# Kernel tuning notes

Hardware: AMD Instinct MI355X
Metric: run time of the kernel (lower is better)

Reference implementation:

```python
import jax, jax.numpy as jnp
import numpy as np

D_MODEL, D_STATE, D_CONV, D_INNER, DT_RANK, K = 96, 16, 3, 192, 6, 4
B, H, W = 1, 64, 64


def setup_inputs() -> dict:
    key = jax.random.key(0)
    ks = jax.random.split(key, 10)
    x = jax.random.normal(ks[0], (B, H, W, D_MODEL), jnp.float32)
    in_proj_w = jax.random.normal(ks[1], (2 * D_INNER, D_MODEL), jnp.float32) * 0.02
    conv_w = jax.random.normal(ks[2], (D_INNER, 1, D_CONV, D_CONV), jnp.float32) * 0.1
    conv_b = jnp.zeros((D_INNER,), jnp.float32)
    x_proj_w = jax.random.normal(ks[3], (K, DT_RANK + 2 * D_STATE, D_INNER), jnp.float32) * 0.02
    dt_std = DT_RANK ** -0.5
    dt_w = jax.random.uniform(ks[4], (K, D_INNER, DT_RANK), jnp.float32, -dt_std, dt_std)
    # dt bias init: inv-softplus of dt ~ logUniform(1e-3, 1e-1)
    u = jax.random.uniform(ks[5], (K, D_INNER), jnp.float32)
    dt = jnp.exp(u * (np.log(0.1) - np.log(0.001)) + np.log(0.001)).clip(1e-4)
    dt_b = dt + jnp.log(-jnp.expm1(-dt))
    A_logs = jnp.log(jnp.broadcast_to(jnp.arange(1, D_STATE + 1, dtype=jnp.float32), (K * D_INNER, D_STATE)))
    Ds = jnp.ones((K * D_INNER,), jnp.float32)
    ln_g = jnp.ones((D_INNER,), jnp.float32)
    ln_b = jnp.zeros((D_INNER,), jnp.float32)
    out_proj_w = jax.random.normal(ks[6], (D_MODEL, D_INNER), jnp.float32) * 0.02
    return dict(x=x, in_proj_w=in_proj_w, conv_w=conv_w, conv_b=conv_b, x_proj_w=x_proj_w,
                dt_w=dt_w, dt_b=dt_b, A_logs=A_logs, Ds=Ds, ln_g=ln_g, ln_b=ln_b,
                out_proj_w=out_proj_w)


def _ss2d(x, in_proj_w, conv_w, conv_b, x_proj_w, dt_w, dt_b, A_logs, Ds, ln_g, ln_b, out_proj_w):
    b, h, w, c = x.shape
    L = h * w
    d = conv_w.shape[0]            # d_inner
    n = A_logs.shape[1]            # d_state
    r = dt_w.shape[2]              # dt_rank
    # in_proj + split
    xz = jnp.einsum('bhwc,ec->bhwe', x, in_proj_w)
    xx, z = xz[..., :d], xz[..., d:]
    # depthwise conv (NCHW) + SiLU
    xc = xx.transpose(0, 3, 1, 2)
    pad = (D_CONV - 1) // 2
    xc = jax.lax.conv_general_dilated(xc, conv_w, (1, 1), [(pad, pad), (pad, pad)],
                                      feature_group_count=d) + conv_b[None, :, None, None]
    xc = jax.nn.silu(xc)
    # 4 scan directions: HW, WH, and their reverses
    x_hw = xc.reshape(b, d, L)
    x_wh = xc.transpose(0, 1, 3, 2).reshape(b, d, L)
    xs = jnp.stack([x_hw, x_wh, x_hw[..., ::-1], x_wh[..., ::-1]], axis=1)  # (b,K,d,L)
    x_dbl = jnp.einsum('bkdl,kcd->bkcl', xs, x_proj_w)
    dts, Bs, Cs = x_dbl[:, :, :r], x_dbl[:, :, r:r + n], x_dbl[:, :, r + n:]
    dts = jnp.einsum('bkrl,kdr->bkdl', dts, dt_w)
    delta = jax.nn.softplus(dts + dt_b[None, :, :, None])        # (b,K,d,L)
    A = -jnp.exp(A_logs).reshape(K, d, n)
    # time-major scanned inputs
    dA = jnp.exp(jnp.einsum('bkdl,kdn->lbkdn', delta, A))        # (L,b,K,d,n)
    dBu = jnp.einsum('bkdl,bknl,bkdl->lbkdn', delta, Bs, xs)
    Ct = Cs.transpose(3, 0, 1, 2)                                # (L,b,K,n)
    def step(hst, inp):
        dA_t, dBu_t, C_t = inp
        hst = dA_t * hst + dBu_t
        return hst, jnp.einsum('bkdn,bkn->bkd', hst, C_t)
    h0 = jnp.zeros((b, K, d, n), jnp.float32)
    _, ys = jax.lax.scan(step, h0, (dA, dBu, Ct))                # ys: (L,b,K,d)
    out_y = ys.transpose(1, 2, 3, 0) + xs * Ds.reshape(K, d)[None, :, :, None]
    # recombine directions
    inv = out_y[:, 2:4][..., ::-1]
    y1 = out_y[:, 0]
    y2 = inv[:, 0]
    wh = out_y[:, 1].reshape(b, d, w, h).transpose(0, 1, 3, 2).reshape(b, d, L)
    invwh = inv[:, 1].reshape(b, d, w, h).transpose(0, 1, 3, 2).reshape(b, d, L)
    y = (y1 + y2 + wh + invwh).transpose(0, 2, 1).reshape(b, h, w, d)
    # LayerNorm (eps=1e-5, torch default)
    mu = y.mean(-1, keepdims=True)
    var = ((y - mu) ** 2).mean(-1, keepdims=True)
    y = (y - mu) * jax.lax.rsqrt(var + 1e-5) * ln_g + ln_b
    y = y * jax.nn.silu(z)
    return jnp.einsum('bhwd,cd->bhwc', y, out_proj_w)


def reference(x, in_proj_w, conv_w, conv_b, x_proj_w, dt_w, dt_b, A_logs, Ds, ln_g, ln_b, out_proj_w):
    return _ss2d(x, in_proj_w, conv_w, conv_b, x_proj_w, dt_w, dt_b, A_logs, Ds, ln_g, ln_b, out_proj_w)
```

## Files before the change

### kernel.cpp

```cpp
#include <hip/hip_runtime.h>
#include <hip/hip_bf16.h>

#define LL 4096
#define DM 96
#define DI 192
#define NS 16
#define RK 6
#define RKP 8
#define KD 4
#define CPROJ 38
#define NC (KD*DI*NS)
#define PT 32
#define WS 196
#define OT 16
#define L2E 1.44269504f

__device__ __forceinline__ float b2f(__hip_bfloat16 v){ return __bfloat162float(v); }

__device__ __forceinline__ int detect_bf16(const unsigned short* __restrict__ xh, int tid, int* sflag){
  if (tid < 64){
    unsigned short u = xh[2*tid];
    int e = (u >> 7) & 0xFF;
    int sane = (e >= 107 && e <= 131) ? 1 : 0;
    unsigned long long m = __ballot(sane);
    if (tid == 0) *sflag = (__popcll(m) >= 32) ? 1 : 0;
  }
  return 0;
}

struct P12 { const void* p[12]; };
__global__ void k_convert_all(P12 ptrs, float* __restrict__ dst) {
  const int off[13] = {0,393216,430080,431808,432000,461184,465792,466560,
                       478848,479616,479808,480000,498432};
  __shared__ int sflag;
  detect_bf16((const unsigned short*)ptrs.p[0], threadIdx.x, &sflag);
  __syncthreads();
  int f = sflag;
  int i = blockIdx.x * 256 + threadIdx.x;
  if (i >= 498432) return;
  int j = 0;
  #pragma unroll
  for (int s = 1; s < 12; s++) if (i >= off[s]) j = s;
  int e = i - off[j];
  if (f) dst[i] = b2f(((const __hip_bfloat16*)ptrs.p[j])[e]);
  else   dst[i] = ((const float*)ptrs.p[j])[e];
}

__global__ void k_inproj(const float* __restrict__ x,
                         const float* __restrict__ w,
                         float* __restrict__ xx, float* __restrict__ z) {
  __shared__ float xr[8*DM];
  int l0 = blockIdx.x * 8;
  int tid = threadIdx.x;
  for (int i = tid; i < 8*DM; i += 384) xr[i] = x[l0*DM + i];
  __syncthreads();
  int e = tid;
  float acc[8];
  #pragma unroll
  for (int i=0;i<8;i++) acc[i]=0.f;
  const float* wr = w + e*DM;
  for (int c=0;c<DM;c++){
    float wv = wr[c];
    #pragma unroll
    for (int i=0;i<8;i++) acc[i] = fmaf(wv, xr[i*DM+c], acc[i]);
  }
  if (e < DI) {
    #pragma unroll
    for (int i=0;i<8;i++) xx[(l0+i)*DI + e] = acc[i];
  } else {
    int e2 = e - DI;
    #pragma unroll
    for (int i=0;i<8;i++) z[(l0+i)*DI + e2] = acc[i];
  }
}

__global__ void k_conv(const float* __restrict__ xx,
                       const float* __restrict__ cw,
                       const float* __restrict__ cb,
                       float* __restrict__ xc) {
  int l = blockIdx.x;
  int d = threadIdx.x;
  int h = l >> 6, w = l & 63;
  float acc = cb[d];
  #pragma unroll
  for (int ki=0; ki<3; ki++){
    int hh = h + ki - 1;
    if ((unsigned)hh >= 64u) continue;
    #pragma unroll
    for (int kj=0;kj<3;kj++){
      int wj = w + kj - 1;
      if ((unsigned)wj >= 64u) continue;
      acc = fmaf(cw[d*9 + ki*3 + kj], xx[(hh*64+wj)*DI + d], acc);
    }
  }
  xc[l*DI + d] = acc / (1.f + __expf(-acc));
}

__device__ __forceinline__ int dir_map(int k, int t){
  if (k==0) return t;
  if (k==1) return ((t&63)<<6) | (t>>6);
  if (k==2) return 4095 - t;
  int u = 4095 - t; return ((u&63)<<6) | (u>>6);
}

__global__ void __launch_bounds__(256) k_proj(const float* __restrict__ xc,
                       const float* __restrict__ xpw,
                       float* __restrict__ dts,
                       float* __restrict__ Bb, float* __restrict__ Cb,
                       float* __restrict__ yacc) {
  __shared__ float wl[CPROJ*WS];
  __shared__ float xs[PT*WS];
  int b = blockIdx.x;
  int k = b >> 7;
  int t_base = (b & 127) * PT;
  int tid = threadIdx.x;
  if (k == 0){
    float4* yz = (float4*)(yacc + (size_t)t_base*DI);
    for (int idx = tid; idx < PT*DI/4; idx += 256)
      yz[idx] = make_float4(0.f,0.f,0.f,0.f);
  }
  for (int idx = tid; idx < CPROJ*DI; idx += 256){
    int cc = idx / DI, j = idx - cc*DI;
    wl[cc*WS + j] = xpw[(k*CPROJ + cc)*DI + j];
  }
  for (int idx = tid; idx < PT*DI; idx += 256){
    int tt = idx / DI, j = idx - tt*DI;
    xs[tt*WS + j] = xc[dir_map(k, t_base + tt)*DI + j];
  }
  __syncthreads();
  int tg = tid & 7;
  int ty = tid >> 3;
  int cc0 = ty;
  int has2 = (ty + 32 < CPROJ);
  int cc1 = has2 ? (ty + 32) : ty;
  float a0x=0.f,a0y=0.f,a0z=0.f,a0w=0.f;
  float a1x=0.f,a1y=0.f,a1z=0.f,a1w=0.f;
  const float4* w0p = (const float4*)&wl[cc0*WS];
  const float4* w1p = (const float4*)&wl[cc1*WS];
  const float4* x0p = (const float4*)&xs[(tg     )*WS];
  const float4* x1p = (const float4*)&xs[(tg +  8)*WS];
  const float4* x2p = (const float4*)&xs[(tg + 16)*WS];
  const float4* x3p = (const float4*)&xs[(tg + 24)*WS];
  #pragma unroll 4
  for (int jc = 0; jc < DI/4; jc++){
    float4 w0 = w0p[jc], w1 = w1p[jc];
    float4 x0 = x0p[jc], x1 = x1p[jc], x2 = x2p[jc], x3 = x3p[jc];
    a0x = fmaf(w0.x,x0.x,fmaf(w0.y,x0.y,fmaf(w0.z,x0.z,fmaf(w0.w,x0.w,a0x))));
    a0y = fmaf(w0.x,x1.x,fmaf(w0.y,x1.y,fmaf(w0.z,x1.z,fmaf(w0.w,x1.w,a0y))));
    a0z = fmaf(w0.x,x2.x,fmaf(w0.y,x2.y,fmaf(w0.z,x2.z,fmaf(w0.w,x2.w,a0z))));
    a0w = fmaf(w0.x,x3.x,fmaf(w0.y,x3.y,fmaf(w0.z,x3.z,fmaf(w0.w,x3.w,a0w))));
    a1x = fmaf(w1.x,x0.x,fmaf(w1.y,x0.y,fmaf(w1.z,x0.z,fmaf(w1.w,x0.w,a1x))));
    a1y = fmaf(w1.x,x1.x,fmaf(w1.y,x1.y,fmaf(w1.z,x1.z,fmaf(w1.w,x1.w,a1y))));
    a1z = fmaf(w1.x,x2.x,fmaf(w1.y,x2.y,fmaf(w1.z,x2.z,fmaf(w1.w,x2.w,a1z))));
    a1w = fmaf(w1.x,x3.x,fmaf(w1.y,x3.y,fmaf(w1.z,x3.z,fmaf(w1.w,x3.w,a1w))));
  }
  float accs0[4] = {a0x,a0y,a0z,a0w};
  float accs1[4] = {a1x,a1y,a1z,a1w};
  #pragma unroll
  for (int i=0;i<4;i++){
    int t = t_base + tg + 8*i;
    size_t kt = (size_t)k*LL + t;
    {
      int cc = cc0; float v = accs0[i];
      if (cc < RK)            dts[kt*RKP + cc] = v;
      else if (cc < RK+NS)    Bb [kt*NS + (cc-RK)] = v;
      else                    Cb [kt*NS + (cc-RK-NS)] = v;
    }
    if (has2){
      int cc = ty + 32; float v = accs1[i];
      if (cc < RK+NS)         Bb [kt*NS + (cc-RK)] = v;
      else                    Cb [kt*NS + (cc-RK-NS)] = v;
    }
  }
}

template<int CHB>
__global__ void __launch_bounds__(256) k_scan1(
                      const float* __restrict__ xc,
                      const float* __restrict__ dts,
                      const float* __restrict__ Bbuf,
                      const float* __restrict__ Cbuf,
                      const float* __restrict__ A_logs,
                      const float* __restrict__ dtw,
                      const float* __restrict__ dtb,
                      float* __restrict__ Pb, float* __restrict__ Hb,
                      float* __restrict__ SDb,
                      float* __restrict__ yacc) {
  constexpr int CS = LL >> CHB;
  int b = blockIdx.x;
  int c = b & ((1<<CHB)-1);
  int kg = b >> CHB;
  int k = kg / 3, dg3 = kg - k*3;
  int tid = threadIdx.x;
  int dl = tid >> 2, nq = tid & 3;
  int d = dg3*64 + dl;
  int kd = k*DI + d;
  float4 Al = *(const float4*)&A_logs[kd*NS + nq*4];
  float A0 = -__expf(Al.x)*L2E, A1 = -__expf(Al.y)*L2E;
  float A2 = -__expf(Al.z)*L2E, A3 = -__expf(Al.w)*L2E;
  float bt = dtb[kd];
  float w0 = dtw[kd*RK+0], w1 = dtw[kd*RK+1], w2 = dtw[kd*RK+2];
  float w3 = dtw[kd*RK+3], w4 = dtw[kd*RK+4], w5 = dtw[kd*RK+5];
  const float* dr = dts + ((size_t)k*LL + c*CS)*RKP;
  const float4* bp = (const float4*)(Bbuf + ((size_t)k*LL + c*CS)*NS) + nq;
  const float4* cp = (const float4*)(Cbuf + ((size_t)k*LL + c*CS)*NS) + nq;
  float h0=0.f,h1=0.f,h2=0.f,h3=0.f, cumD=0.f;
  for (int s=0; s<CS; s++){
    int t = c*CS + s;
    float4 lo = *(const float4*)(dr + s*RKP);
    float4 hi = *(const float4*)(dr + s*RKP + 4);
    float v = bt;
    v = fmaf(w0, lo.x, v); v = fmaf(w1, lo.y, v); v = fmaf(w2, lo.z, v);
    v = fmaf(w3, lo.w, v); v = fmaf(w4, hi.x, v); v = fmaf(w5, hi.y, v);
    float sp = (v > 20.f) ? v : __logf(1.f + __expf(v));
    cumD += sp;
    int l = dir_map(k,t);
    float sx = sp * xc[l*DI + d];
    float4 bv = bp[s*4];
    float4 cv = cp[s*4];
    float a;
    a = exp2f(sp*A0); h0 = fmaf(a, h0, sx*bv.x);
    a = exp2f(sp*A1); h1 = fmaf(a, h1, sx*bv.y);
    a = exp2f(sp*A2); h2 = fmaf(a, h2, sx*bv.z);
    a = exp2f(sp*A3); h3 = fmaf(a, h3, sx*bv.w);
    float y = h0*cv.x + h1*cv.y + h2*cv.z + h3*cv.w;
    y += __shfl_xor(y, 1, 64);
    y += __shfl_xor(y, 2, 64);
    if (nq == 0){
      atomicAdd(&yacc[(size_t)l*DI + d], y);
      SDb[(size_t)(k*LL + t)*DI + d] = cumD;
    }
  }
  int base = c*NC + kd*NS + nq*4;
  *(float4*)&Pb[base] = make_float4(exp2f(A0*cumD), exp2f(A1*cumD),
                                    exp2f(A2*cumD), exp2f(A3*cumD));
  *(float4*)&Hb[base] = make_float4(h0,h1,h2,h3);
}

__global__ void __launch_bounds__(256) k_scan2(
                      const float* __restrict__ Pb, float* __restrict__ Hb,
                      int CHn) {
  int idx = blockIdx.x*256 + threadIdx.x;
  float h = 0.f;
  #pragma unroll 4
  for (int c=0;c<CHn;c++){
    float P = Pb[c*NC + idx];
    float Hc = Hb[c*NC + idx];
    Hb[c*NC + idx] = h;
    h = fmaf(P, h, Hc);
  }
}

template<int CHB>
__global__ void __launch_bounds__(192) k_corr(
                      const float* __restrict__ Cbuf,
                      const float* __restrict__ A_logs,
                      const float* __restrict__ Hb,
                      const float* __restrict__ SDb,
                      float* __restrict__ yacc) {
  int b = blockIdx.x;
  int k = b >> 7;
  int t0 = (b & 127) * 32;
  int c = t0 >> (12 - CHB);
  if (c == 0) return;
  int d = threadIdx.x;
  int kd = k*DI + d;
  __shared__ float cs[32*NS];
  for (int i = d; i < 32*NS; i += 192)
    cs[i] = Cbuf[((size_t)k*LL + t0)*NS + i];
  float A2[16], he[16];
  {
    const float4* ap = (const float4*)&A_logs[kd*NS];
    const float4* hp = (const float4*)&Hb[c*NC + kd*NS];
    #pragma unroll
    for (int i=0;i<4;i++){
      float4 av = ap[i];
      A2[4*i+0] = -__expf(av.x)*L2E; A2[4*i+1] = -__expf(av.y)*L2E;
      A2[4*i+2] = -__expf(av.z)*L2E; A2[4*i+3] = -__expf(av.w)*L2E;
      *(float4*)&he[4*i] = hp[i];
    }
  }
  __syncthreads();
  for (int s=0; s<32; s++){
    int t = t0 + s;
    float SD = SDb[(size_t)(k*LL + t)*DI + d];
    float corr = 0.f;
    #pragma unroll
    for (int n=0;n<16;n++)
      corr = fmaf(cs[s*NS+n]*exp2f(A2[n]*SD), he[n], corr);
    atomicAdd(&yacc[(size_t)dir_map(k,t)*DI + d], corr);
  }
}

__global__ void k_ln(const float* __restrict__ yacc,
                     const float* __restrict__ xc,
                     const float* __restrict__ z,
                     const float* __restrict__ Ds,
                     const float* __restrict__ ln_g,
                     const float* __restrict__ ln_b,
                     float* __restrict__ g) {
  int l = blockIdx.x;
  int d = threadIdx.x;
  float y = yacc[(size_t)l*DI + d];
  float dsum = Ds[0*DI+d] + Ds[1*DI+d] + Ds[2*DI+d] + Ds[3*DI+d];
  y = fmaf(xc[l*DI+d], dsum, y);
  float s1 = y, s2 = y*y;
  #pragma unroll
  for (int off=32; off; off>>=1){
    s1 += __shfl_xor(s1, off, 64);
    s2 += __shfl_xor(s2, off, 64);
  }
  __shared__ float red[6];
  int wave = d >> 6;
  if ((d & 63) == 0){ red[wave] = s1; red[3+wave] = s2; }
  __syncthreads();
  float sum = red[0]+red[1]+red[2];
  float sq  = red[3]+red[4]+red[5];
  float mu = sum * (1.f/192.f);
  float var = sq * (1.f/192.f) - mu*mu;
  float rstd = rsqrtf(var + 1e-5f);
  float yn = (y - mu) * rstd * ln_g[d] + ln_b[d];
  float zv = z[l*DI + d];
  g[(size_t)l*DI + d] = yn * (zv / (1.f + __expf(-zv)));
}

__global__ void __launch_bounds__(192) k_oproj(const float* __restrict__ g,
                      const float* __restrict__ opw,
                      void* __restrict__ out,
                      const unsigned short* __restrict__ xh) {
  __shared__ float gs[OT*WS];
  __shared__ int sflag;
  int tid = threadIdx.x;
  detect_bf16(xh, tid, &sflag);
  int l0 = blockIdx.x * OT;
  const float4* gsrc = (const float4*)(g + (size_t)l0*DI);
  for (int idx = tid; idx < OT*DI/4; idx += 192){
    int row = idx / 48, col = idx - row*48;
    float4 v = gsrc[idx];
    *(float4*)&gs[row*WS + col*4] = v;
  }
  __syncthreads();
  int half = tid / 96;
  int e = tid - half*96;
  int r0 = half*8;
  float acc[8];
  #pragma unroll
  for (int i=0;i<8;i++) acc[i] = 0.f;
  const float4* wrow = (const float4*)(opw + e*DI);
  #pragma unroll 4
  for (int jc = 0; jc < DI/4; jc++){
    float4 w = wrow[jc];
    #pragma unroll
    for (int i=0;i<8;i++){
      float4 gv = *(const float4*)&gs[(r0+i)*WS + jc*4];
      acc[i] = fmaf(w.x,gv.x,fmaf(w.y,gv.y,fmaf(w.z,gv.z,fmaf(w.w,gv.w,acc[i]))));
    }
  }
  int f = sflag;
  #pragma unroll
  for (int i=0;i<8;i++){
    int l = l0 + r0 + i;
    if (f) ((__hip_bfloat16*)out)[l*DM + e] = __float2bfloat16(acc[i]);
    else   ((float*)out)[l*DM + e] = acc[i];
  }
}

extern "C" void kernel_launch(void* const* d_in, const int* in_sizes, int n_in,
                              void* d_out, int out_size, void* d_ws, size_t ws_size,
                              hipStream_t stream) {
  float* ws = (float*)d_ws;
  float* cvt = ws + 16;
  const int off[13] = {0,393216,430080,431808,432000,461184,465792,466560,
                       478848,479616,479808,480000,498432};
  float* c[12];
  for (int i = 0; i < 12; i++) c[i] = cvt + off[i];

  float* big    = cvt + 498432;
  float* xx     = big;
  float* z      = xx + (size_t)LL*DI;
  float* xc     = z  + (size_t)LL*DI;
  float* dts    = xc + (size_t)LL*DI;
  float* Bb     = dts + (size_t)KD*LL*RKP;
  float* Cb     = Bb + (size_t)KD*LL*NS;
  float* Pb     = Cb + (size_t)KD*LL*NS;
  size_t need128 = (size_t)(16 + 498432 + 3*786432 + 131072 + 2*262144
                            + 2*128*NC + (size_t)KD*LL*DI) * 4;
  int chBits = (ws_size >= need128) ? 7 : 6;
  int CHn = 1 << chBits;
  float* Hb   = Pb + (size_t)CHn*NC;
  float* SDb  = Hb + (size_t)CHn*NC;
  float* yacc = xx;

  P12 ptrs;
  for (int i = 0; i < 12; i++) ptrs.p[i] = d_in[i];
  k_convert_all<<<(498432 + 255)/256, 256, 0, stream>>>(ptrs, cvt);

  k_inproj<<<LL/8, 384, 0, stream>>>(c[0], c[1], xx, z);
  k_conv<<<LL, DI, 0, stream>>>(xx, c[2], c[3], xc);
  k_proj<<<KD*(LL/PT), 256, 0, stream>>>(xc, c[4], dts, Bb, Cb, yacc);
  if (chBits == 7){
    k_scan1<7><<<KD*3*128, 256, 0, stream>>>(xc, dts, Bb, Cb, c[7], c[5], c[6], Pb, Hb, SDb, yacc);
    k_scan2<<<NC/256, 256, 0, stream>>>(Pb, Hb, 128);
    k_corr<7><<<KD*128, 192, 0, stream>>>(Cb, c[7], Hb, SDb, yacc);
  } else {
    k_scan1<6><<<KD*3*64, 256, 0, stream>>>(xc, dts, Bb, Cb, c[7], c[5], c[6], Pb, Hb, SDb, yacc);
    k_scan2<<<NC/256, 256, 0, stream>>>(Pb, Hb, 64);
    k_corr<6><<<KD*128, 192, 0, stream>>>(Cb, c[7], Hb, SDb, yacc);
  }
  k_ln<<<LL, DI, 0, stream>>>(yacc, xc, z, c[8], c[9], c[10], Hb);
  k_oproj<<<LL/OT, 192, 0, stream>>>(Hb, c[11], d_out, (const unsigned short*)d_in[0]);
}
```

Measured before the change: 216.8 us.

## Add transposed conv output and split accumulators for contiguous scan access

The conv kernel now also writes a transposed (W-major) copy of its output, so the WH-direction scans read x and accumulate y with a constant stride instead of scattered dir_map indexing. Output accumulation is split into separate HW and WH buffers that are recombined in the LayerNorm kernel. The chunked scan goes from 128 to 256 chunks for more parallelism, and k_corr is restructured to one block per chunk. This costs extra workspace, an extra transposed write, and a longer sequential chunk-combine pass in k_scan2.

```diff
diff --git a/kernel.cpp b/kernel.cpp
--- a/kernel.cpp
+++ b/kernel.cpp
@@ -77,7 +77,8 @@
 __global__ void k_conv(const float* __restrict__ xx,
                        const float* __restrict__ cw,
                        const float* __restrict__ cb,
-                       float* __restrict__ xc) {
+                       float* __restrict__ xc,
+                       float* __restrict__ xct) {
   int l = blockIdx.x;
   int d = threadIdx.x;
   int h = l >> 6, w = l & 63;
@@ -93,7 +94,9 @@
       acc = fmaf(cw[d*9 + ki*3 + kj], xx[(hh*64+wj)*DI + d], acc);
     }
   }
-  xc[l*DI + d] = acc / (1.f + __expf(-acc));
+  float v = acc / (1.f + __expf(-acc));
+  xc[l*DI + d] = v;
+  xct[(((w<<6)|h))*DI + d] = v;
 }
 
 __device__ __forceinline__ int dir_map(int k, int t){
@@ -107,15 +110,15 @@
                        const float* __restrict__ xpw,
                        float* __restrict__ dts,
                        float* __restrict__ Bb, float* __restrict__ Cb,
-                       float* __restrict__ yacc) {
+                       float* __restrict__ yacc_hw, float* __restrict__ yacc_wh) {
   __shared__ float wl[CPROJ*WS];
   __shared__ float xs[PT*WS];
   int b = blockIdx.x;
   int k = b >> 7;
   int t_base = (b & 127) * PT;
   int tid = threadIdx.x;
-  if (k == 0){
-    float4* yz = (float4*)(yacc + (size_t)t_base*DI);
+  if (k < 2){
+    float4* yz = (float4*)((k==0 ? yacc_hw : yacc_wh) + (size_t)t_base*DI);
     for (int idx = tid; idx < PT*DI/4; idx += 256)
       yz[idx] = make_float4(0.f,0.f,0.f,0.f);
   }
@@ -176,7 +179,8 @@
 
 template<int CHB>
 __global__ void __launch_bounds__(256) k_scan1(
-                      const float* __restrict__ xc,
+                      const float* __restrict__ xc_hw,
+                      const float* __restrict__ xc_wh,
                       const float* __restrict__ dts,
                       const float* __restrict__ Bbuf,
                       const float* __restrict__ Cbuf,
@@ -185,7 +189,7 @@
                       const float* __restrict__ dtb,
                       float* __restrict__ Pb, float* __restrict__ Hb,
                       float* __restrict__ SDb,
-                      float* __restrict__ yacc) {
+                      float* __restrict__ yacc_hw, float* __restrict__ yacc_wh) {
   constexpr int CS = LL >> CHB;
   int b = blockIdx.x;
   int c = b & ((1<<CHB)-1);
@@ -204,9 +208,16 @@
   const float* dr = dts + ((size_t)k*LL + c*CS)*RKP;
   const float4* bp = (const float4*)(Bbuf + ((size_t)k*LL + c*CS)*NS) + nq;
   const float4* cp = (const float4*)(Cbuf + ((size_t)k*LL + c*CS)*NS) + nq;
+  const float* xbase = (k & 1) ? xc_wh : xc_hw;
+  float* ybase = (k & 1) ? yacc_wh : yacc_hw;
+  int l0 = (k < 2) ? (c*CS) : (4095 - c*CS);
+  int lstep = (k < 2) ? DI : -DI;
+  const float* xp = xbase + (size_t)l0*DI + d;
+  float* yp = ybase + (size_t)l0*DI + d;
+  float* sdp = SDb + ((size_t)k*LL + c*CS)*DI + d;
   float h0=0.f,h1=0.f,h2=0.f,h3=0.f, cumD=0.f;
+  #pragma unroll
   for (int s=0; s<CS; s++){
-    int t = c*CS + s;
     float4 lo = *(const float4*)(dr + s*RKP);
     float4 hi = *(const float4*)(dr + s*RKP + 4);
     float v = bt;
@@ -214,8 +225,7 @@
     v = fmaf(w3, lo.w, v); v = fmaf(w4, hi.x, v); v = fmaf(w5, hi.y, v);
     float sp = (v > 20.f) ? v : __logf(1.f + __expf(v));
     cumD += sp;
-    int l = dir_map(k,t);
-    float sx = sp * xc[l*DI + d];
+    float sx = sp * xp[(ptrdiff_t)s*lstep];
     float4 bv = bp[s*4];
     float4 cv = cp[s*4];
     float a;
@@ -227,8 +237,8 @@
     y += __shfl_xor(y, 1, 64);
     y += __shfl_xor(y, 2, 64);
     if (nq == 0){
-      atomicAdd(&yacc[(size_t)l*DI + d], y);
-      SDb[(size_t)(k*LL + t)*DI + d] = cumD;
+      atomicAdd(&yp[(ptrdiff_t)s*lstep], y);
+      sdp[s*DI] = cumD;
     }
   }
   int base = c*NC + kd*NS + nq*4;
@@ -237,13 +247,14 @@
   *(float4*)&Hb[base] = make_float4(h0,h1,h2,h3);
 }
 
+template<int CHB>
 __global__ void __launch_bounds__(256) k_scan2(
-                      const float* __restrict__ Pb, float* __restrict__ Hb,
-                      int CHn) {
+                      const float* __restrict__ Pb, float* __restrict__ Hb) {
+  constexpr int CH = 1 << CHB;
   int idx = blockIdx.x*256 + threadIdx.x;
   float h = 0.f;
-  #pragma unroll 4
-  for (int c=0;c<CHn;c++){
+  #pragma unroll 8
+  for (int c=0;c<CH;c++){
     float P = Pb[c*NC + idx];
     float Hc = Hb[c*NC + idx];
     Hb[c*NC + idx] = h;
@@ -257,16 +268,17 @@
                       const float* __restrict__ A_logs,
                       const float* __restrict__ Hb,
                       const float* __restrict__ SDb,
-                      float* __restrict__ yacc) {
+                      float* __restrict__ yacc_hw, float* __restrict__ yacc_wh) {
+  constexpr int CS = LL >> CHB;
   int b = blockIdx.x;
-  int k = b >> 7;
-  int t0 = (b & 127) * 32;
-  int c = t0 >> (12 - CHB);
+  int k = b >> CHB;
+  int c = b & ((1<<CHB)-1);
   if (c == 0) return;
+  int t0 = c*CS;
   int d = threadIdx.x;
   int kd = k*DI + d;
-  __shared__ float cs[32*NS];
-  for (int i = d; i < 32*NS; i += 192)
+  __shared__ float cs[CS*NS];
+  for (int i = d; i < CS*NS; i += 192)
     cs[i] = Cbuf[((size_t)k*LL + t0)*NS + i];
   float A2[16], he[16];
   {
@@ -281,18 +293,24 @@
     }
   }
   __syncthreads();
-  for (int s=0; s<32; s++){
-    int t = t0 + s;
-    float SD = SDb[(size_t)(k*LL + t)*DI + d];
+  float* ybase = (k & 1) ? yacc_wh : yacc_hw;
+  int l0 = (k < 2) ? t0 : (4095 - t0);
+  int lstep = (k < 2) ? DI : -DI;
+  float* yp = ybase + (size_t)l0*DI + d;
+  const float* sdp = SDb + ((size_t)k*LL + t0)*DI + d;
+  #pragma unroll 4
+  for (int s=0; s<CS; s++){
+    float SD = sdp[s*DI];
     float corr = 0.f;
     #pragma unroll
     for (int n=0;n<16;n++)
       corr = fmaf(cs[s*NS+n]*exp2f(A2[n]*SD), he[n], corr);
-    atomicAdd(&yacc[(size_t)dir_map(k,t)*DI + d], corr);
-  }
-}
-
-__global__ void k_ln(const float* __restrict__ yacc,
+    atomicAdd(&yp[(ptrdiff_t)s*lstep], corr);
+  }
+}
+
+__global__ void k_ln(const float* __restrict__ yacc_hw,
+                     const float* __restrict__ yacc_wh,
                      const float* __restrict__ xc,
                      const float* __restrict__ z,
                      const float* __restrict__ Ds,
@@ -301,7 +319,8 @@
                      float* __restrict__ g) {
   int l = blockIdx.x;
   int d = threadIdx.x;
-  float y = yacc[(size_t)l*DI + d];
+  int lt = ((l & 63) << 6) | (l >> 6);
+  float y = yacc_hw[(size_t)l*DI + d] + yacc_wh[(size_t)lt*DI + d];
   float dsum = Ds[0*DI+d] + Ds[1*DI+d] + Ds[2*DI+d] + Ds[3*DI+d];
   y = fmaf(xc[l*DI+d], dsum, y);
   float s1 = y, s2 = y*y;
@@ -379,34 +398,38 @@
   float* xx     = big;
   float* z      = xx + (size_t)LL*DI;
   float* xc     = z  + (size_t)LL*DI;
-  float* dts    = xc + (size_t)LL*DI;
+  float* xct    = xc + (size_t)LL*DI;
+  float* dts    = xct + (size_t)LL*DI;
   float* Bb     = dts + (size_t)KD*LL*RKP;
   float* Cb     = Bb + (size_t)KD*LL*NS;
   float* Pb     = Cb + (size_t)KD*LL*NS;
-  size_t need128 = (size_t)(16 + 498432 + 3*786432 + 131072 + 2*262144
-                            + 2*128*NC + (size_t)KD*LL*DI) * 4;
-  int chBits = (ws_size >= need128) ? 7 : 6;
+  size_t need256 = (size_t)(16 + 498432 + 4*786432 + 131072 + 2*262144
+                            + 2*256*NC + (size_t)KD*LL*DI + 786432) * 4;
+  int chBits = (ws_size >= need256) ? 8 : 6;
   int CHn = 1 << chBits;
-  float* Hb   = Pb + (size_t)CHn*NC;
-  float* SDb  = Hb + (size_t)CHn*NC;
-  float* yacc = xx;
+  float* Hb      = Pb + (size_t)CHn*NC;
+  float* SDb     = Hb + (size_t)CHn*NC;
+  float* yacc_wh = SDb + (size_t)KD*LL*DI;
+  float* yacc_hw = xx;
 
   P12 ptrs;
   for (int i = 0; i < 12; i++) ptrs.p[i] = d_in[i];
   k_convert_all<<<(498432 + 255)/256, 256, 0, stream>>>(ptrs, cvt);
 
   k_inproj<<<LL/8, 384, 0, stream>>>(c[0], c[1], xx, z);
-  k_conv<<<LL, DI, 0, stream>>>(xx, c[2], c[3], xc);
-  k_proj<<<KD*(LL/PT), 256, 0, stream>>>(xc, c[4], dts, Bb, Cb, yacc);
-  if (chBits == 7){
-    k_scan1<7><<<KD*3*128, 256, 0, stream>>>(xc, dts, Bb, Cb, c[7], c[5], c[6], Pb, Hb, SDb, yacc);
-    k_scan2<<<NC/256, 256, 0, stream>>>(Pb, Hb, 128);
-    k_corr<7><<<KD*128, 192, 0, stream>>>(Cb, c[7], Hb, SDb, yacc);
+  k_conv<<<LL, DI, 0, stream>>>(xx, c[2], c[3], xc, xct);
+  k_proj<<<KD*(LL/PT), 256, 0, stream>>>(xc, c[4], dts, Bb, Cb, yacc_hw, yacc_wh);
+  if (chBits == 8){
+    k_scan1<8><<<KD*3*256, 256, 0, stream>>>(xc, xct, dts, Bb, Cb, c[7], c[5], c[6],
+                                             Pb, Hb, SDb, yacc_hw, yacc_wh);
+    k_scan2<8><<<NC/256, 256, 0, stream>>>(Pb, Hb);
+    k_corr<8><<<KD*256, 192, 0, stream>>>(Cb, c[7], Hb, SDb, yacc_hw, yacc_wh);
   } else {
-    k_scan1<6><<<KD*3*64, 256, 0, stream>>>(xc, dts, Bb, Cb, c[7], c[5], c[6], Pb, Hb, SDb, yacc);
-    k_scan2<<<NC/256, 256, 0, stream>>>(Pb, Hb, 64);
-    k_corr<6><<<KD*128, 192, 0, stream>>>(Cb, c[7], Hb, SDb, yacc);
-  }
-  k_ln<<<LL, DI, 0, stream>>>(yacc, xc, z, c[8], c[9], c[10], Hb);
+    k_scan1<6><<<KD*3*64, 256, 0, stream>>>(xc, xct, dts, Bb, Cb, c[7], c[5], c[6],
+                                            Pb, Hb, SDb, yacc_hw, yacc_wh);
+    k_scan2<6><<<NC/256, 256, 0, stream>>>(Pb, Hb);
+    k_corr<6><<<KD*64, 192, 0, stream>>>(Cb, c[7], Hb, SDb, yacc_hw, yacc_wh);
+  }
+  k_ln<<<LL, DI, 0, stream>>>(yacc_hw, yacc_wh, xc, z, c[8], c[9], c[10], Hb);
   k_oproj<<<LL/OT, 192, 0, stream>>>(Hb, c[11], d_out, (const unsigned short*)d_in[0]);
 }
```

After: 207.8 us. -4.1%, faster.
